# Optimization experiments

Hardware: AMD Instinct MI355X
Metric: run time of the kernel (lower is better)

## Reference

```python
import jax, jax.numpy as jnp
import numpy as np

B, S, H, NH = 2, 2048, 1024, 16
HD = H // NH  # 64
EPS = 1e-5


def setup_inputs() -> dict:
    key = jax.random.key(0)
    ks = jax.random.split(key, 4)
    return {
        "hidden_states": jax.random.normal(ks[0], (B, S, H), dtype=jnp.float32),
        "W_attn": jax.random.normal(ks[1], (H, 3 * H), dtype=jnp.float32) * (1.0 / np.sqrt(H)),
        "b_attn": jnp.zeros((3 * H,), dtype=jnp.float32),
        "W_proj": jax.random.normal(ks[2], (H, H), dtype=jnp.float32) * (1.0 / np.sqrt(H)),
        "b_proj": jnp.zeros((H,), dtype=jnp.float32),
        "q_gamma": jnp.ones((HD,), dtype=jnp.float32),
        "q_beta": jnp.zeros((HD,), dtype=jnp.float32),
        "k_gamma": jnp.ones((HD,), dtype=jnp.float32),
        "k_beta": jnp.zeros((HD,), dtype=jnp.float32),
    }


def _layernorm(x, gamma, beta):
    mu = jnp.mean(x, axis=-1, keepdims=True)
    var = jnp.mean(jnp.square(x - mu), axis=-1, keepdims=True)
    return (x - mu) * jax.lax.rsqrt(var + EPS) * gamma + beta


def reference(hidden_states, W_attn, b_attn, W_proj, b_proj, q_gamma, q_beta, k_gamma, k_beta):
    b, s, h = hidden_states.shape
    qkv = hidden_states @ W_attn + b_attn  # [B,S,3H]
    q, k, v = jnp.split(qkv, 3, axis=-1)
    # [B,S,H] -> [B,NH,S,HD]
    def to_heads(t):
        return t.reshape(b, s, NH, HD).transpose(0, 2, 1, 3)
    q, k, v = to_heads(q), to_heads(k), to_heads(v)
    # QK LayerNorm over head_dim
    q = _layernorm(q, q_gamma, q_beta)
    k = _layernorm(k, k_gamma, k_beta)
    scale = HD ** (-0.5)
    scores = jnp.einsum("bhqd,bhkd->bhqk", q, k) * scale
    causal = jnp.tril(jnp.ones((s, s), dtype=bool))
    mask_value = jnp.finfo(scores.dtype).min
    scores = jnp.where(causal, scores, mask_value)
    attn = jax.nn.softmax(scores.astype(jnp.float32), axis=-1).astype(q.dtype)
    out = jnp.einsum("bhqk,bhkd->bhqd", attn, v)
    out = out.transpose(0, 2, 1, 3).reshape(b, s, h)
    out = out @ W_proj + b_proj
    return out
```

## Files before the change

### kernel.cpp

```cpp
#include <hip/hip_runtime.h>
#include <hip/hip_bf16.h>

typedef __bf16 bf16x8 __attribute__((ext_vector_type(8)));
typedef float f32x4 __attribute__((ext_vector_type(4)));

#define EPS 1e-5f
#define QSCALE 0.18033688011112042f

__device__ __forceinline__ unsigned short f2bf(float f) {
  union { float f; unsigned int i; } c; c.f = f;
  unsigned int r = c.i + 0x7FFFu + ((c.i >> 16) & 1u);
  return (unsigned short)(r >> 16);
}
__device__ __forceinline__ unsigned short f2bf_t(float f) {
  union { float f; unsigned int i; } c; c.f = f;
  return (unsigned short)(c.i >> 16);
}

__device__ __forceinline__ void glds16(const void* g, void* l) {
  __builtin_amdgcn_global_load_lds(
      (const __attribute__((address_space(1))) unsigned int*)g,
      (__attribute__((address_space(3))) unsigned int*)l, 16, 0, 0);
}

__device__ __forceinline__ void transpose_tile(
    const float* __restrict__ in, unsigned short* __restrict__ out,
    int R, int C, int ct0, int rt0, unsigned short* S )
{
  const int t = threadIdx.x;
  const int r = t >> 2, c4 = (t & 3) * 16;
  {
    long base = (long)(rt0 + r) * C + ct0 + c4;
    float4 a = *(const float4*)&in[base];
    float4 b = *(const float4*)&in[base + 4];
    float4 c = *(const float4*)&in[base + 8];
    float4 d = *(const float4*)&in[base + 12];
    unsigned short v[16] = {f2bf(a.x), f2bf(a.y), f2bf(a.z), f2bf(a.w),
                            f2bf(b.x), f2bf(b.y), f2bf(b.z), f2bf(b.w),
                            f2bf(c.x), f2bf(c.y), f2bf(c.z), f2bf(c.w),
                            f2bf(d.x), f2bf(d.y), f2bf(d.z), f2bf(d.w)};
    *(uint4*)&S[r * 72 + c4]     = *(uint4*)&v[0];
    *(uint4*)&S[r * 72 + c4 + 8] = *(uint4*)&v[8];
  }
  __syncthreads();
  unsigned short tmp[16];
#pragma unroll
  for (int j = 0; j < 16; j++) tmp[j] = S[(c4 + j) * 72 + r];
  *(uint4*)&out[(long)(ct0 + r) * R + rt0 + c4]     = *(uint4*)&tmp[0];
  *(uint4*)&out[(long)(ct0 + r) * R + rt0 + c4 + 8] = *(uint4*)&tmp[8];
}

__global__ __launch_bounds__(256) void prep_kernel(
    const float* __restrict__ Wa, const float* __restrict__ Wp,
    const float* __restrict__ X,
    unsigned short* __restrict__ WaT, unsigned short* __restrict__ WpT,
    unsigned short* __restrict__ Xbf)
{
  __shared__ __align__(16) unsigned short S[64 * 72];
  const int id = blockIdx.x;
  if (id < 768) {
    transpose_tile(Wa, WaT, 1024, 3072, (id % 48) * 64, (id / 48) * 64, S);
  } else if (id < 1024) {
    const int i2 = id - 768;
    transpose_tile(Wp, WpT, 1024, 1024, (i2 % 16) * 64, (i2 / 16) * 64, S);
  } else {
    long i = ((long)(id - 1024) * 256 + threadIdx.x) * 16;
    float4 a = *(const float4*)&X[i];
    float4 b = *(const float4*)&X[i + 4];
    float4 c = *(const float4*)&X[i + 8];
    float4 d = *(const float4*)&X[i + 12];
    unsigned short v[16] = {f2bf(a.x), f2bf(a.y), f2bf(a.z), f2bf(a.w),
                            f2bf(b.x), f2bf(b.y), f2bf(b.z), f2bf(b.w),
                            f2bf(c.x), f2bf(c.y), f2bf(c.z), f2bf(c.w),
                            f2bf(d.x), f2bf(d.y), f2bf(d.z), f2bf(d.w)};
    *(uint4*)&Xbf[i]     = *(uint4*)&v[0];
    *(uint4*)&Xbf[i + 8] = *(uint4*)&v[8];
  }
}

__global__ __launch_bounds__(256) void qkvt_kernel(
    const float* __restrict__ Xf,
    const unsigned short* __restrict__ Xbf, int use_xbf,
    const unsigned short* __restrict__ WT,
    const float* __restrict__ bias,
    const float* __restrict__ qg, const float* __restrict__ qb,
    const float* __restrict__ kg, const float* __restrict__ kb,
    unsigned short* __restrict__ Qws, unsigned short* __restrict__ Kws,
    unsigned short* __restrict__ Vt)
{
  __shared__ __align__(16) unsigned short As[2][128 * 32];
  __shared__ __align__(16) unsigned short Bs[2][128 * 32];

  const int tid = threadIdx.x;
  const int w = tid >> 6, lane = tid & 63, quad = lane >> 4, l15 = lane & 15;
  const int mh = w & 1, nh = w >> 1;
  const int id = blockIdx.x;
  const int grow = lane >> 2, gcol = (lane & 3) * 8;

  if (id < 512) {
    const int n0 = (id & 15) * 128, m0 = (id >> 4) * 128;

    f32x4 acc[4][4];
#pragma unroll
    for (int i = 0; i < 4; i++)
#pragma unroll
      for (int j = 0; j < 4; j++) acc[i][j] = (f32x4){0.f, 0.f, 0.f, 0.f};

    if (use_xbf) {
      const long ga = (long)(m0 + w * 32 + grow) * 1024 + gcol;
      const long gb = (long)(n0 + w * 32 + grow) * 1024 + gcol;
#define STAGE_QK(bf, kk) do { \
        glds16(&Xbf[ga + (kk)],             &As[bf][(w * 32) * 32]); \
        glds16(&Xbf[ga + (kk) + 16 * 1024], &As[bf][(w * 32 + 16) * 32]); \
        glds16(&WT[gb + (kk)],              &Bs[bf][(w * 32) * 32]); \
        glds16(&WT[gb + (kk) + 16 * 1024],  &Bs[bf][(w * 32 + 16) * 32]); \
      } while (0)
      STAGE_QK(0, 0);
      __syncthreads();
      int buf = 0;
      for (int kt = 0; kt < 1024; kt += 32) {
        if (kt + 32 < 1024) STAGE_QK(buf ^ 1, kt + 32);
        bf16x8 af[4], bfr[4];
#pragma unroll
        for (int mq = 0; mq < 4; mq++)
          af[mq] = *(const bf16x8*)&As[buf][(mh * 64 + mq * 16 + l15) * 32 + quad * 8];
#pragma unroll
        for (int nq = 0; nq < 4; nq++)
          bfr[nq] = *(const bf16x8*)&Bs[buf][(nh * 64 + nq * 16 + l15) * 32 + quad * 8];
#pragma unroll
        for (int mq = 0; mq < 4; mq++)
#pragma unroll
          for (int nq = 0; nq < 4; nq++)
            acc[mq][nq] = __builtin_amdgcn_mfma_f32_16x16x32_bf16(af[mq], bfr[nq], acc[mq][nq], 0, 0, 0);
        __syncthreads();
        buf ^= 1;
      }
#undef STAGE_QK
    } else {
      const int sr2 = tid >> 1, sh2 = (tid & 1) * 16;
      {
        long xo = (long)(m0 + sr2) * 1024 + sh2;
        float4 a0 = *(const float4*)&Xf[xo];
        float4 a1 = *(const float4*)&Xf[xo + 4];
        float4 a2 = *(const float4*)&Xf[xo + 8];
        float4 a3 = *(const float4*)&Xf[xo + 12];
        unsigned short v[16] = {f2bf(a0.x), f2bf(a0.y), f2bf(a0.z), f2bf(a0.w),
                                f2bf(a1.x), f2bf(a1.y), f2bf(a1.z), f2bf(a1.w),
                                f2bf(a2.x), f2bf(a2.y), f2bf(a2.z), f2bf(a2.w),
                                f2bf(a3.x), f2bf(a3.y), f2bf(a3.z), f2bf(a3.w)};
        *(uint4*)&As[0][sr2 * 32 + sh2]     = *(uint4*)&v[0];
        *(uint4*)&As[0][sr2 * 32 + sh2 + 8] = *(uint4*)&v[8];
        long wo = (long)(n0 + sr2) * 1024 + sh2;
        *(uint4*)&Bs[0][sr2 * 32 + sh2]     = *(const uint4*)&WT[wo];
        *(uint4*)&Bs[0][sr2 * 32 + sh2 + 8] = *(const uint4*)&WT[wo + 8];
      }
      __syncthreads();

      int buf = 0;
      for (int kt = 0; kt < 1024; kt += 32) {
        const int nbuf = buf ^ 1;
        const bool pf = (kt + 32) < 1024;
        uint4 wv0, wv1;
        float4 a0, a1, a2, a3;
        if (pf) {
          long xo = (long)(m0 + sr2) * 1024 + kt + 32 + sh2;
          a0 = *(const float4*)&Xf[xo];
          a1 = *(const float4*)&Xf[xo + 4];
          a2 = *(const float4*)&Xf[xo + 8];
          a3 = *(const float4*)&Xf[xo + 12];
          long wo = (long)(n0 + sr2) * 1024 + kt + 32 + sh2;
          wv0 = *(const uint4*)&WT[wo];
          wv1 = *(const uint4*)&WT[wo + 8];
        }

        bf16x8 af[4], bfr[4];
#pragma unroll
        for (int mq = 0; mq < 4; mq++)
          af[mq] = *(const bf16x8*)&As[buf][(mh * 64 + mq * 16 + l15) * 32 + quad * 8];
#pragma unroll
        for (int nq = 0; nq < 4; nq++)
          bfr[nq] = *(const bf16x8*)&Bs[buf][(nh * 64 + nq * 16 + l15) * 32 + quad * 8];
#pragma unroll
        for (int mq = 0; mq < 4; mq++)
#pragma unroll
          for (int nq = 0; nq < 4; nq++)
            acc[mq][nq] = __builtin_amdgcn_mfma_f32_16x16x32_bf16(af[mq], bfr[nq], acc[mq][nq], 0, 0, 0);

        if (pf) {
          unsigned short v[16] = {f2bf(a0.x), f2bf(a0.y), f2bf(a0.z), f2bf(a0.w),
                                  f2bf(a1.x), f2bf(a1.y), f2bf(a1.z), f2bf(a1.w),
                                  f2bf(a2.x), f2bf(a2.y), f2bf(a2.z), f2bf(a2.w),
                                  f2bf(a3.x), f2bf(a3.y), f2bf(a3.z), f2bf(a3.w)};
          *(uint4*)&As[nbuf][sr2 * 32 + sh2]     = *(uint4*)&v[0];
          *(uint4*)&As[nbuf][sr2 * 32 + sh2 + 8] = *(uint4*)&v[8];
          *(uint4*)&Bs[nbuf][sr2 * 32 + sh2]     = wv0;
          *(uint4*)&Bs[nbuf][sr2 * 32 + sh2 + 8] = wv1;
        }
        __syncthreads();
        buf = nbuf;
      }
    }

#pragma unroll
    for (int nq = 0; nq < 4; nq++) {
      float bv = bias[n0 + nh * 64 + nq * 16 + l15];
#pragma unroll
      for (int mq = 0; mq < 4; mq++)
#pragma unroll
        for (int rr = 0; rr < 4; rr++) acc[mq][nq][rr] += bv;
    }

    const int g = (n0 >> 6) + nh;
    const bool isQ = g < 16;
    {
      float gv[4], bev[4];
#pragma unroll
      for (int nq = 0; nq < 4; nq++) {
        int d = nq * 16 + l15;
        gv[nq]  = isQ ? qg[d] : kg[d];
        bev[nq] = isQ ? qb[d] : kb[d];
        if (isQ) { gv[nq] *= QSCALE; bev[nq] *= QSCALE; }
      }
#pragma unroll
      for (int mq = 0; mq < 4; mq++)
#pragma unroll
        for (int rr = 0; rr < 4; rr++) {
          float s  = acc[mq][0][rr] + acc[mq][1][rr] + acc[mq][2][rr] + acc[mq][3][rr];
          float s2 = acc[mq][0][rr]*acc[mq][0][rr] + acc[mq][1][rr]*acc[mq][1][rr]
                   + acc[mq][2][rr]*acc[mq][2][rr] + acc[mq][3][rr]*acc[mq][3][rr];
#pragma unroll
          for (int off = 1; off < 16; off <<= 1) {
            s  += __shfl_xor(s,  off, 64);
            s2 += __shfl_xor(s2, off, 64);
          }
          float mu   = s * (1.0f / 64.0f);
          float var  = fmaxf(s2 * (1.0f / 64.0f) - mu * mu, 0.f);
          float rstd = rsqrtf(var + EPS);
#pragma unroll
          for (int nq = 0; nq < 4; nq++)
            acc[mq][nq][rr] = (acc[mq][nq][rr] - mu) * rstd * gv[nq] + bev[nq];
        }
    }

    unsigned short* dst = isQ ? Qws : Kws;
    const int head = isQ ? g : g - 16;
#pragma unroll
    for (int mq = 0; mq < 4; mq++)
#pragma unroll
      for (int rr = 0; rr < 4; rr++) {
        int m = m0 + mh * 64 + mq * 16 + quad * 4 + rr;
        int b = m >> 11, s = m & 2047;
        long base = ((long)((b * 16 + head) * 2048 + s)) * 64;
#pragma unroll
        for (int nq = 0; nq < 4; nq++)
          dst[base + nq * 16 + l15] = f2bf(acc[mq][nq][rr]);
      }
  } else {
    const int id2 = id - 512;
    const int n0 = (id2 & 31) * 64, m0 = ((id2 >> 5) & 7) * 128, bz = id2 >> 8;
    const long xrow0 = (long)bz * 2048;
    const unsigned short* WvT = WT + 2048L * 1024;

    f32x4 acc[4][2];
#pragma unroll
    for (int i = 0; i < 4; i++)
#pragma unroll
      for (int j = 0; j < 2; j++) acc[i][j] = (f32x4){0.f, 0.f, 0.f, 0.f};

    if (use_xbf) {
      const long gva = (long)(m0 + w * 32 + grow) * 1024 + gcol;
      const long gvb = (xrow0 + n0 + w * 16 + grow) * 1024 + gcol;
#define STAGE_V(bf, kk) do { \
        glds16(&WvT[gva + (kk)],             &As[bf][(w * 32) * 32]); \
        glds16(&WvT[gva + (kk) + 16 * 1024], &As[bf][(w * 32 + 16) * 32]); \
        glds16(&Xbf[gvb + (kk)],             &Bs[bf][(w * 16) * 32]); \
      } while (0)
      STAGE_V(0, 0);
      __syncthreads();
      int buf = 0;
      for (int kt = 0; kt < 1024; kt += 32) {
        if (kt + 32 < 1024) STAGE_V(buf ^ 1, kt + 32);
        bf16x8 af[4], bfr[2];
#pragma unroll
        for (int mq = 0; mq < 4; mq++)
          af[mq] = *(const bf16x8*)&As[buf][(mh * 64 + mq * 16 + l15) * 32 + quad * 8];
#pragma unroll
        for (int nq = 0; nq < 2; nq++)
          bfr[nq] = *(const bf16x8*)&Bs[buf][(nh * 32 + nq * 16 + l15) * 32 + quad * 8];
#pragma unroll
        for (int mq = 0; mq < 4; mq++)
#pragma unroll
          for (int nq = 0; nq < 2; nq++)
            acc[mq][nq] = __builtin_amdgcn_mfma_f32_16x16x32_bf16(af[mq], bfr[nq], acc[mq][nq], 0, 0, 0);
        __syncthreads();
        buf ^= 1;
      }
#undef STAGE_V
    } else {
      const int srA = tid >> 1, shA = (tid & 1) * 16;
      const int srB = tid >> 2, shB = (tid & 3) * 8;
      {
        long wo = (long)(m0 + srA) * 1024 + shA;
        *(uint4*)&As[0][srA * 32 + shA]     = *(const uint4*)&WvT[wo];
        *(uint4*)&As[0][srA * 32 + shA + 8] = *(const uint4*)&WvT[wo + 8];
        long xo = (xrow0 + n0 + srB) * 1024 + shB;
        float4 a0 = *(const float4*)&Xf[xo];
        float4 a1 = *(const float4*)&Xf[xo + 4];
        unsigned short v[8] = {f2bf(a0.x), f2bf(a0.y), f2bf(a0.z), f2bf(a0.w),
                               f2bf(a1.x), f2bf(a1.y), f2bf(a1.z), f2bf(a1.w)};
        *(uint4*)&Bs[0][srB * 32 + shB] = *(uint4*)v;
      }
      __syncthreads();

      int buf = 0;
      for (int kt = 0; kt < 1024; kt += 32) {
        const int nbuf = buf ^ 1;
        const bool pf = (kt + 32) < 1024;
        uint4 wv0, wv1;
        float4 a0, a1;
        if (pf) {
          long wo = (long)(m0 + srA) * 1024 + kt + 32 + shA;
          wv0 = *(const uint4*)&WvT[wo];
          wv1 = *(const uint4*)&WvT[wo + 8];
          long xo = (xrow0 + n0 + srB) * 1024 + kt + 32 + shB;
          a0 = *(const float4*)&Xf[xo];
          a1 = *(const float4*)&Xf[xo + 4];
        }

        bf16x8 af[4], bfr[2];
#pragma unroll
        for (int mq = 0; mq < 4; mq++)
          af[mq] = *(const bf16x8*)&As[buf][(mh * 64 + mq * 16 + l15) * 32 + quad * 8];
#pragma unroll
        for (int nq = 0; nq < 2; nq++)
          bfr[nq] = *(const bf16x8*)&Bs[buf][(nh * 32 + nq * 16 + l15) * 32 + quad * 8];
#pragma unroll
        for (int mq = 0; mq < 4; mq++)
#pragma unroll
          for (int nq = 0; nq < 2; nq++)
            acc[mq][nq] = __builtin_amdgcn_mfma_f32_16x16x32_bf16(af[mq], bfr[nq], acc[mq][nq], 0, 0, 0);

        if (pf) {
          *(uint4*)&As[nbuf][srA * 32 + shA]     = wv0;
          *(uint4*)&As[nbuf][srA * 32 + shA + 8] = wv1;
          unsigned short v[8] = {f2bf(a0.x), f2bf(a0.y), f2bf(a0.z), f2bf(a0.w),
                                 f2bf(a1.x), f2bf(a1.y), f2bf(a1.z), f2bf(a1.w)};
          *(uint4*)&Bs[nbuf][srB * 32 + shB] = *(uint4*)v;
        }
        __syncthreads();
        buf = nbuf;
      }
    }

    const long outb = (long)bz * 2097152;
#pragma unroll
    for (int mq = 0; mq < 4; mq++)
#pragma unroll
      for (int rr = 0; rr < 4; rr++) {
        int m = m0 + mh * 64 + mq * 16 + quad * 4 + rr;
        float bv = bias[2048 + m];
#pragma unroll
        for (int nq = 0; nq < 2; nq++) {
          int n = n0 + nh * 32 + nq * 16 + l15;
          Vt[outb + (long)m * 2048 + n] = f2bf(acc[mq][nq][rr] + bv);
        }
      }
  }
}

__global__ __launch_bounds__(512) void attn_kernel(
    unsigned short* __restrict__ Qws,
    const unsigned short* __restrict__ Kws,
    const unsigned short* __restrict__ Vt)
{
  __shared__ __align__(16) unsigned short Ks[2][64 * 72];
  __shared__ __align__(16) unsigned short VTs[2][64 * 72];
  __shared__ __align__(16) unsigned short Ps[2][64 * 64];

  const int tid = threadIdx.x;
  const int w = tid >> 6, lane = tid & 63, quad = lane >> 4, l15 = lane & 15;
  const int g = w >> 2, wq = w & 3;
  const int id = blockIdx.x;
  const int bh = (id & 7) * 4 + ((id >> 3) & 3);
  const int i5 = id >> 5;
  const int x  = (i5 < 8) ? i5 : 23 - i5;
  const long bhoff = (long)bh * 2048 * 64;
  const long bhv   = (long)bh * 131072;

  const int qt_long = 31 - x;
  const int myqt  = g ? x : qt_long;
  const int qbase = myqt * 64;
  const int jsteps = qt_long + 1;

  const int t2 = tid & 255;
  const int sr = t2 >> 2, sc = (t2 & 3) * 16;
  const int qsw = ((sr >> 2) & 3) << 4;
  const int sw = ((l15 >> 2) & 3) << 4;
  const int pc0 = (quad * 8) ^ sw;
  const int pc1 = (32 + quad * 8) ^ sw;

  bf16x8 ones;
  {
    union { unsigned short u[8]; bf16x8 v; } c;
#pragma unroll
    for (int i = 0; i < 8; i++) c.u[i] = 0x3F80u;
    ones = c.v;
  }

  *(uint4*)&Ps[g][sr * 64 + (sc ^ qsw)]       = *(const uint4*)&Qws[bhoff + (qbase + sr) * 64 + sc];
  *(uint4*)&Ps[g][sr * 64 + ((sc ^ qsw) + 8)] = *(const uint4*)&Qws[bhoff + (qbase + sr) * 64 + sc + 8];
  if (g == 0) {
    *(uint4*)&Ks[0][sr * 72 + sc]      = *(const uint4*)&Kws[bhoff + sr * 64 + sc];
    *(uint4*)&Ks[0][sr * 72 + sc + 8]  = *(const uint4*)&Kws[bhoff + sr * 64 + sc + 8];
  } else {
    *(uint4*)&VTs[0][sr * 72 + sc]     = *(const uint4*)&Vt[bhv + sr * 2048 + sc];
    *(uint4*)&VTs[0][sr * 72 + sc + 8] = *(const uint4*)&Vt[bhv + sr * 2048 + sc + 8];
  }
  __syncthreads();

  const bf16x8 qf0 = *(const bf16x8*)&Ps[g][(wq * 16 + l15) * 64 + pc0];
  const bf16x8 qf1 = *(const bf16x8*)&Ps[g][(wq * 16 + l15) * 64 + pc1];

  f32x4 o[4], osum;
#pragma unroll
  for (int i = 0; i < 4; i++) o[i] = (f32x4){0.f, 0.f, 0.f, 0.f};
  osum = (f32x4){0.f, 0.f, 0.f, 0.f};

  int cb = 0;
  for (int j = 0; j < jsteps; j++) {
    const int kb = j * 64;
    const bool pf = (j + 1) < jsteps;
    uint4 p0, p1;
    if (pf) {
      const int kb1 = kb + 64;
      if (g == 0) {
        p0 = *(const uint4*)&Kws[bhoff + (kb1 + sr) * 64 + sc];
        p1 = *(const uint4*)&Kws[bhoff + (kb1 + sr) * 64 + sc + 8];
      } else {
        p0 = *(const uint4*)&Vt[bhv + sr * 2048 + kb1 + sc];
        p1 = *(const uint4*)&Vt[bhv + sr * 2048 + kb1 + sc + 8];
      }
    }

    if (j <= myqt) {
      f32x4 sacc[4];
#pragma unroll
      for (int i = 0; i < 4; i++) sacc[i] = (f32x4){0.f, 0.f, 0.f, 0.f};
#pragma unroll
      for (int nt = 0; nt < 4; nt++) {
        bf16x8 kf0 = *(const bf16x8*)&Ks[cb][(nt * 16 + l15) * 72 + quad * 8];
        bf16x8 kf1 = *(const bf16x8*)&Ks[cb][(nt * 16 + l15) * 72 + 32 + quad * 8];
        sacc[nt] = __builtin_amdgcn_mfma_f32_16x16x32_bf16(qf0, kf0, sacc[nt], 0, 0, 0);
        sacc[nt] = __builtin_amdgcn_mfma_f32_16x16x32_bf16(qf1, kf1, sacc[nt], 0, 0, 0);
      }

      const bool domask = (j == myqt);
#pragma unroll
      for (int nt = 0; nt < 4; nt++)
#pragma unroll
        for (int rr = 0; rr < 4; rr++) {
          float p = exp2f(sacc[nt][rr]);
          if (domask) {
            int kcol = kb + nt * 16 + l15;
            int qrow = qbase + wq * 16 + quad * 4 + rr;
            if (kcol > qrow) p = 0.f;
          }
          sacc[nt][rr] = p;
        }

#pragma unroll
      for (int rr = 0; rr < 4; rr++)
#pragma unroll
        for (int nt = 0; nt < 4; nt++)
          Ps[g][(wq * 16 + quad * 4 + rr) * 64 + (((nt ^ quad) & 3) * 16 + l15)]
              = f2bf_t(sacc[nt][rr]);

      bf16x8 pfr0 = *(const bf16x8*)&Ps[g][(wq * 16 + l15) * 64 + pc0];
      bf16x8 pfr1 = *(const bf16x8*)&Ps[g][(wq * 16 + l15) * 64 + pc1];

      osum = __builtin_amdgcn_mfma_f32_16x16x32_bf16(pfr0, ones, osum, 0, 0, 0);
      osum = __builtin_amdgcn_mfma_f32_16x16x32_bf16(pfr1, ones, osum, 0, 0, 0);
#pragma unroll
      for (int dt = 0; dt < 4; dt++) {
        bf16x8 vf0 = *(const bf16x8*)&VTs[cb][(dt * 16 + l15) * 72 + quad * 8];
        bf16x8 vf1 = *(const bf16x8*)&VTs[cb][(dt * 16 + l15) * 72 + 32 + quad * 8];
        o[dt] = __builtin_amdgcn_mfma_f32_16x16x32_bf16(pfr0, vf0, o[dt], 0, 0, 0);
        o[dt] = __builtin_amdgcn_mfma_f32_16x16x32_bf16(pfr1, vf1, o[dt], 0, 0, 0);
      }
    }

    if (pf) {
      const int nb = cb ^ 1;
      if (g == 0) {
        *(uint4*)&Ks[nb][sr * 72 + sc]      = p0;
        *(uint4*)&Ks[nb][sr * 72 + sc + 8]  = p1;
      } else {
        *(uint4*)&VTs[nb][sr * 72 + sc]     = p0;
        *(uint4*)&VTs[nb][sr * 72 + sc + 8] = p1;
      }
      __syncthreads();
      cb = nb;
    }
  }

#pragma unroll
  for (int rr = 0; rr < 4; rr++) {
    float inv = 1.0f / osum[rr];
    int row = qbase + wq * 16 + quad * 4 + rr;
    long base = bhoff + (long)row * 64;
#pragma unroll
    for (int dt = 0; dt < 4; dt++)
      Qws[base + dt * 16 + l15] = f2bf(o[dt][rr] * inv);
  }
}

__global__ __launch_bounds__(256) void proj_kernel(
    const unsigned short* __restrict__ AQ,
    const unsigned short* __restrict__ WT,
    const float* __restrict__ bias,
    float* __restrict__ Out)
{
  __shared__ __align__(16) unsigned short As[2][128 * 32];
  __shared__ __align__(16) unsigned short Bs[2][64 * 32];

  const int tid = threadIdx.x;
  const int w = tid >> 6, lane = tid & 63, quad = lane >> 4, l15 = lane & 15;
  const int mh = w & 1, nh = w >> 1;
  const int n0 = blockIdx.x * 64, m0 = blockIdx.y * 128;

  f32x4 acc[4][2];
#pragma unroll
  for (int i = 0; i < 4; i++)
#pragma unroll
    for (int j = 0; j < 2; j++) acc[i][j] = (f32x4){0.f, 0.f, 0.f, 0.f};

  const int srA = tid >> 1, shA = (tid & 1) * 16;
  const int srB = tid >> 2, shB = (tid & 3) * 8;
  const int m = m0 + srA, b = m >> 11, s = m & 2047;

  {
    const int h = shA >> 6, d = shA & 63;
    long ao = ((long)((b * 16 + h) * 2048 + s)) * 64 + d;
    *(uint4*)&As[0][srA * 32 + shA]     = *(const uint4*)&AQ[ao];
    *(uint4*)&As[0][srA * 32 + shA + 8] = *(const uint4*)&AQ[ao + 8];
    long wo = (long)(n0 + srB) * 1024 + shB;
    *(uint4*)&Bs[0][srB * 32 + shB] = *(const uint4*)&WT[wo];
  }
  __syncthreads();

  int buf = 0;
  for (int kt = 0; kt < 1024; kt += 32) {
    const int nbuf = buf ^ 1;
    const bool pf = (kt + 32) < 1024;
    uint4 av0, av1, wv0;
    if (pf) {
      const int k = kt + 32 + shA, h = k >> 6, d = k & 63;
      long ao = ((long)((b * 16 + h) * 2048 + s)) * 64 + d;
      av0 = *(const uint4*)&AQ[ao];
      av1 = *(const uint4*)&AQ[ao + 8];
      long wo = (long)(n0 + srB) * 1024 + kt + 32 + shB;
      wv0 = *(const uint4*)&WT[wo];
    }

    bf16x8 af[4], bfr[2];
#pragma unroll
    for (int mq = 0; mq < 4; mq++)
      af[mq] = *(const bf16x8*)&As[buf][(mh * 64 + mq * 16 + l15) * 32 + quad * 8];
#pragma unroll
    for (int nq = 0; nq < 2; nq++)
      bfr[nq] = *(const bf16x8*)&Bs[buf][(nh * 32 + nq * 16 + l15) * 32 + quad * 8];
#pragma unroll
    for (int mq = 0; mq < 4; mq++)
#pragma unroll
      for (int nq = 0; nq < 2; nq++)
        acc[mq][nq] = __builtin_amdgcn_mfma_f32_16x16x32_bf16(af[mq], bfr[nq], acc[mq][nq], 0, 0, 0);

    if (pf) {
      *(uint4*)&As[nbuf][srA * 32 + shA]     = av0;
      *(uint4*)&As[nbuf][srA * 32 + shA + 8] = av1;
      *(uint4*)&Bs[nbuf][srB * 32 + shB]     = wv0;
    }
    __syncthreads();
    buf = nbuf;
  }

#pragma unroll
  for (int nq = 0; nq < 2; nq++) {
    int n = n0 + nh * 32 + nq * 16 + l15;
    float bv = bias[n];
#pragma unroll
    for (int mq = 0; mq < 4; mq++)
#pragma unroll
      for (int rr = 0; rr < 4; rr++) {
        int mm = m0 + mh * 64 + mq * 16 + quad * 4 + rr;
        Out[(long)mm * 1024 + n] = acc[mq][nq][rr] + bv;
      }
  }
}

extern "C" void kernel_launch(void* const* d_in, const int* in_sizes, int n_in,
                              void* d_out, int out_size, void* d_ws, size_t ws_size,
                              hipStream_t stream) {
  const float* X  = (const float*)d_in[0];
  const float* Wa = (const float*)d_in[1];
  const float* ba = (const float*)d_in[2];
  const float* Wp = (const float*)d_in[3];
  const float* bp = (const float*)d_in[4];
  const float* qg = (const float*)d_in[5];
  const float* qb = (const float*)d_in[6];
  const float* kg = (const float*)d_in[7];
  const float* kb = (const float*)d_in[8];

  const long per = 2L * 16 * 2048 * 64;
  unsigned short* ws  = (unsigned short*)d_ws;
  unsigned short* Qws = ws;
  unsigned short* Kws = Qws + per;
  unsigned short* Vt  = Kws + per;

  const bool big = ws_size >= (size_t)(5L * per * 2);
  unsigned short *Xbf, *WaT, *WpT;
  if (big) {
    Xbf = Vt + per;
    WaT = Xbf + per;
    WpT = WaT + 3072L * 1024;
  } else {
    Xbf = Qws;
    WaT = Vt + per;
    WpT = WaT + 3072L * 1024;
  }

  prep_kernel<<<big ? 2048 : 1024, 256, 0, stream>>>(Wa, Wp, X, WaT, WpT, Xbf);
  qkvt_kernel<<<1024, 256, 0, stream>>>(X, Xbf, big ? 1 : 0, WaT, ba,
                                        qg, qb, kg, kb, Qws, Kws, Vt);
  attn_kernel<<<512, 512, 0, stream>>>(Qws, Kws, Vt);
  proj_kernel<<<dim3(16, 32), 256, 0, stream>>>(Qws, WpT, bp, (float*)d_out);
}
```

Measured before the change: 205.9 us.

## Add 256x256-tile 8-wave QKV GEMM with swizzled LDS and XCD-aware block mapping

Adds a new QKV projection kernel for the big-workspace path. It uses 256x256 output tiles, 512 threads, K-steps of 64, and direct global-to-LDS loads with XOR-swizzled LDS addresses. MFMA work is split into phases interleaved with prefetches, using explicit waitcnt and barriers plus s_setprio. Block IDs are remapped so neighbouring tiles land on the same XCD, and proj_kernel gets the same XCD-aware 1D mapping. The aim is more operand reuse, fewer LDS bank conflicts and better L2 locality, at the cost of a large LDS footprint (128KB) and occupancy of one block per CU.

```diff
diff --git a/kernel.cpp b/kernel.cpp
--- a/kernel.cpp
+++ b/kernel.cpp
@@ -78,9 +78,221 @@
   }
 }
 
+__global__ __launch_bounds__(512) void qkvt8_kernel(
+    const unsigned short* __restrict__ Xbf,
+    const unsigned short* __restrict__ WT,
+    const float* __restrict__ bias,
+    const float* __restrict__ qg, const float* __restrict__ qb,
+    const float* __restrict__ kg, const float* __restrict__ kb,
+    unsigned short* __restrict__ Qws, unsigned short* __restrict__ Kws,
+    unsigned short* __restrict__ Vt)
+{
+  __shared__ __align__(16) unsigned short As[2][256 * 64];
+  __shared__ __align__(16) unsigned short Bs[2][256 * 64];
+
+  const int tid = threadIdx.x;
+  const int wv = tid >> 6, lane = tid & 63, quad = lane >> 4, l15 = lane & 15;
+  const int wm = wv >> 2, wn = wv & 3;
+  const int id = blockIdx.x;
+
+  const unsigned short *Abase, *Bbase;
+  int m0, n0, bz = 0;
+  bool isV;
+  if (id < 128) {
+    const int xcd = id & 7, lid = id >> 3;
+    m0 = (((xcd >> 1) << 2) + (lid >> 2)) * 256;
+    n0 = (((xcd & 1) << 2) + (lid & 3)) * 256;
+    Abase = Xbf; Bbase = WT; isV = false;
+  } else {
+    const int vid = id - 128, xcd = vid & 7, lid2 = vid >> 3;
+    bz = xcd >> 2;
+    n0 = (((xcd & 3) << 1) + (lid2 & 1)) * 256;
+    m0 = (lid2 >> 1) * 256;
+    Abase = WT + 2048L * 1024;
+    Bbase = Xbf + (long)bz * 2048 * 1024;
+    isV = true;
+  }
+
+  const int gsw  = ((lane & 7) ^ (((lane >> 5) & 1) << 1)) * 8;
+  const int grow = lane >> 3;
+  const int rsw = (l15 & 4) >> 1;
+  const int co0 = ((0 + quad) ^ rsw) * 8;
+  const int co1 = ((4 + quad) ^ rsw) * 8;
+
+#define STG_A(BUF, H, KK) do { \
+    const int L0_ = wv * 2, L1_ = L0_ + 1; \
+    const int r0_ = ((L0_ >> 3) << 7) + (H) * 64 + ((L0_ & 7) << 3); \
+    const int r1_ = ((L1_ >> 3) << 7) + (H) * 64 + ((L1_ & 7) << 3); \
+    glds16(&Abase[(long)(m0 + r0_ + grow) * 1024 + (KK) + gsw], &As[BUF][r0_ * 64]); \
+    glds16(&Abase[(long)(m0 + r1_ + grow) * 1024 + (KK) + gsw], &As[BUF][r1_ * 64]); \
+  } while (0)
+#define STG_B(BUF, H, KK) do { \
+    const int L0_ = wv * 2, L1_ = L0_ + 1; \
+    const int r0_ = ((L0_ >> 2) << 6) + (H) * 32 + ((L0_ & 3) << 3); \
+    const int r1_ = ((L1_ >> 2) << 6) + (H) * 32 + ((L1_ & 3) << 3); \
+    glds16(&Bbase[(long)(n0 + r0_ + grow) * 1024 + (KK) + gsw], &Bs[BUF][r0_ * 64]); \
+    glds16(&Bbase[(long)(n0 + r1_ + grow) * 1024 + (KK) + gsw], &Bs[BUF][r1_ * 64]); \
+  } while (0)
+#define LDA4(BUF, MQB) \
+  _Pragma("unroll") \
+  for (int q = 0; q < 4; q++) { \
+    const int r_ = (wm * 128 + ((MQB) + q) * 16 + l15) * 64; \
+    a[q][0] = *(const bf16x8*)&As[BUF][r_ + co0]; \
+    a[q][1] = *(const bf16x8*)&As[BUF][r_ + co1]; \
+  }
+#define LDB2(BUF, NQB, DST) \
+  _Pragma("unroll") \
+  for (int q = 0; q < 2; q++) { \
+    const int r_ = (wn * 64 + ((NQB) + q) * 16 + l15) * 64; \
+    DST[q][0] = *(const bf16x8*)&Bs[BUF][r_ + co0]; \
+    DST[q][1] = *(const bf16x8*)&Bs[BUF][r_ + co1]; \
+  }
+#define MMQ(MQB, NQB, BV) \
+  __builtin_amdgcn_s_setprio(1); \
+  _Pragma("unroll") \
+  for (int qi = 0; qi < 4; qi++) \
+    _Pragma("unroll") \
+    for (int qj = 0; qj < 2; qj++) { \
+      acc[(MQB) + qi][(NQB) + qj] = __builtin_amdgcn_mfma_f32_16x16x32_bf16( \
+          a[qi][0], BV[qj][0], acc[(MQB) + qi][(NQB) + qj], 0, 0, 0); \
+      acc[(MQB) + qi][(NQB) + qj] = __builtin_amdgcn_mfma_f32_16x16x32_bf16( \
+          a[qi][1], BV[qj][1], acc[(MQB) + qi][(NQB) + qj], 0, 0, 0); \
+    } \
+  __builtin_amdgcn_s_setprio(0)
+#define PH_MID() do { __builtin_amdgcn_s_barrier(); \
+    asm volatile("s_waitcnt lgkmcnt(0)" ::: "memory"); } while (0)
+#define PH_END() __builtin_amdgcn_s_barrier()
+
+  f32x4 acc[8][4];
+#pragma unroll
+  for (int i = 0; i < 8; i++)
+#pragma unroll
+    for (int j = 0; j < 4; j++) acc[i][j] = (f32x4){0.f, 0.f, 0.f, 0.f};
+
+  STG_A(0, 0, 0); STG_B(0, 0, 0); STG_B(0, 1, 0); STG_A(0, 1, 0);
+  STG_A(1, 0, 64); STG_B(1, 0, 64); STG_B(1, 1, 64);
+  asm volatile("s_waitcnt vmcnt(6)" ::: "memory");
+  __builtin_amdgcn_s_barrier();
+
+  for (int it = 0; it < 8; it++) {
+    const int k1 = it * 128 + 64;
+    const int k2 = it * 128 + 128;
+    const int k3 = it * 128 + 192;
+    const bool pf = (it < 7);
+    bf16x8 a[4][2], b01[2][2], b23[2][2];
+
+    LDA4(0, 0) LDB2(0, 0, b01)
+    STG_A(1, 1, k1);
+    PH_MID(); MMQ(0, 0, b01); PH_END();
+    LDB2(0, 2, b23)
+    if (pf) STG_A(0, 0, k2);
+    PH_MID(); MMQ(0, 2, b23); PH_END();
+    LDA4(0, 4)
+    if (pf) STG_B(0, 0, k2);
+    PH_MID(); MMQ(4, 2, b23); PH_END();
+    if (pf) { STG_B(0, 1, k2);
+      asm volatile("s_waitcnt vmcnt(6)" ::: "memory");
+    } else {
+      asm volatile("s_waitcnt vmcnt(0)" ::: "memory");
+    }
+    PH_MID(); MMQ(4, 0, b01); PH_END();
+
+    LDA4(1, 0) LDB2(1, 0, b01)
+    if (pf) STG_A(0, 1, k2);
+    PH_MID(); MMQ(0, 0, b01); PH_END();
+    LDB2(1, 2, b23)
+    if (pf) STG_A(1, 0, k3);
+    PH_MID(); MMQ(0, 2, b23); PH_END();
+    LDA4(1, 4)
+    if (pf) STG_B(1, 0, k3);
+    PH_MID(); MMQ(4, 2, b23); PH_END();
+    if (pf) { STG_B(1, 1, k3);
+      asm volatile("s_waitcnt vmcnt(6)" ::: "memory");
+    } else {
+      asm volatile("s_waitcnt vmcnt(0)" ::: "memory");
+    }
+    PH_MID(); MMQ(4, 0, b01); PH_END();
+  }
+#undef STG_A
+#undef STG_B
+#undef LDA4
+#undef LDB2
+#undef MMQ
+#undef PH_MID
+#undef PH_END
+
+  if (!isV) {
+#pragma unroll
+    for (int nq = 0; nq < 4; nq++) {
+      float bv = bias[n0 + wn * 64 + nq * 16 + l15];
+#pragma unroll
+      for (int mq = 0; mq < 8; mq++)
+#pragma unroll
+        for (int rr = 0; rr < 4; rr++) acc[mq][nq][rr] += bv;
+    }
+
+    const int g = (n0 >> 6) + wn;
+    const bool isQ = g < 16;
+    float gv[4], bev[4];
+#pragma unroll
+    for (int nq = 0; nq < 4; nq++) {
+      int d = nq * 16 + l15;
+      gv[nq]  = isQ ? qg[d] : kg[d];
+      bev[nq] = isQ ? qb[d] : kb[d];
+      if (isQ) { gv[nq] *= QSCALE; bev[nq] *= QSCALE; }
+    }
+#pragma unroll
+    for (int mq = 0; mq < 8; mq++)
+#pragma unroll
+      for (int rr = 0; rr < 4; rr++) {
+        float s  = acc[mq][0][rr] + acc[mq][1][rr] + acc[mq][2][rr] + acc[mq][3][rr];
+        float s2 = acc[mq][0][rr]*acc[mq][0][rr] + acc[mq][1][rr]*acc[mq][1][rr]
+                 + acc[mq][2][rr]*acc[mq][2][rr] + acc[mq][3][rr]*acc[mq][3][rr];
+#pragma unroll
+        for (int off = 1; off < 16; off <<= 1) {
+          s  += __shfl_xor(s,  off, 64);
+          s2 += __shfl_xor(s2, off, 64);
+        }
+        float mu   = s * (1.0f / 64.0f);
+        float var  = fmaxf(s2 * (1.0f / 64.0f) - mu * mu, 0.f);
+        float rstd = rsqrtf(var + EPS);
+#pragma unroll
+        for (int nq = 0; nq < 4; nq++)
+          acc[mq][nq][rr] = (acc[mq][nq][rr] - mu) * rstd * gv[nq] + bev[nq];
+      }
+
+    unsigned short* dst = isQ ? Qws : Kws;
+    const int head = isQ ? g : g - 16;
+#pragma unroll
+    for (int mq = 0; mq < 8; mq++)
+#pragma unroll
+      for (int rr = 0; rr < 4; rr++) {
+        int m = m0 + wm * 128 + mq * 16 + quad * 4 + rr;
+        int b = m >> 11, s = m & 2047;
+        long base = ((long)((b * 16 + head) * 2048 + s)) * 64;
+#pragma unroll
+        for (int nq = 0; nq < 4; nq++)
+          dst[base + nq * 16 + l15] = f2bf(acc[mq][nq][rr]);
+      }
+  } else {
+    const long outb = (long)bz * 2097152;
+#pragma unroll
+    for (int mq = 0; mq < 8; mq++)
+#pragma unroll
+      for (int rr = 0; rr < 4; rr++) {
+        int m = m0 + wm * 128 + mq * 16 + quad * 4 + rr;
+        float bv = bias[2048 + m];
+#pragma unroll
+        for (int nq = 0; nq < 4; nq++) {
+          int n = n0 + wn * 64 + nq * 16 + l15;
+          Vt[outb + (long)m * 2048 + n] = f2bf(acc[mq][nq][rr] + bv);
+        }
+      }
+  }
+}
+
 __global__ __launch_bounds__(256) void qkvt_kernel(
     const float* __restrict__ Xf,
-    const unsigned short* __restrict__ Xbf, int use_xbf,
     const unsigned short* __restrict__ WT,
     const float* __restrict__ bias,
     const float* __restrict__ qg, const float* __restrict__ qb,
@@ -95,110 +307,74 @@
   const int w = tid >> 6, lane = tid & 63, quad = lane >> 4, l15 = lane & 15;
   const int mh = w & 1, nh = w >> 1;
   const int id = blockIdx.x;
-  const int grow = lane >> 2, gcol = (lane & 3) * 8;
 
   if (id < 512) {
     const int n0 = (id & 15) * 128, m0 = (id >> 4) * 128;
-
     f32x4 acc[4][4];
 #pragma unroll
     for (int i = 0; i < 4; i++)
 #pragma unroll
       for (int j = 0; j < 4; j++) acc[i][j] = (f32x4){0.f, 0.f, 0.f, 0.f};
 
-    if (use_xbf) {
-      const long ga = (long)(m0 + w * 32 + grow) * 1024 + gcol;
-      const long gb = (long)(n0 + w * 32 + grow) * 1024 + gcol;
-#define STAGE_QK(bf, kk) do { \
-        glds16(&Xbf[ga + (kk)],             &As[bf][(w * 32) * 32]); \
-        glds16(&Xbf[ga + (kk) + 16 * 1024], &As[bf][(w * 32 + 16) * 32]); \
-        glds16(&WT[gb + (kk)],              &Bs[bf][(w * 32) * 32]); \
-        glds16(&WT[gb + (kk) + 16 * 1024],  &Bs[bf][(w * 32 + 16) * 32]); \
-      } while (0)
-      STAGE_QK(0, 0);
-      __syncthreads();
-      int buf = 0;
-      for (int kt = 0; kt < 1024; kt += 32) {
-        if (kt + 32 < 1024) STAGE_QK(buf ^ 1, kt + 32);
-        bf16x8 af[4], bfr[4];
-#pragma unroll
-        for (int mq = 0; mq < 4; mq++)
-          af[mq] = *(const bf16x8*)&As[buf][(mh * 64 + mq * 16 + l15) * 32 + quad * 8];
+    const int sr2 = tid >> 1, sh2 = (tid & 1) * 16;
+    {
+      long xo = (long)(m0 + sr2) * 1024 + sh2;
+      float4 a0 = *(const float4*)&Xf[xo];
+      float4 a1 = *(const float4*)&Xf[xo + 4];
+      float4 a2 = *(const float4*)&Xf[xo + 8];
+      float4 a3 = *(const float4*)&Xf[xo + 12];
+      unsigned short v[16] = {f2bf(a0.x), f2bf(a0.y), f2bf(a0.z), f2bf(a0.w),
+                              f2bf(a1.x), f2bf(a1.y), f2bf(a1.z), f2bf(a1.w),
+                              f2bf(a2.x), f2bf(a2.y), f2bf(a2.z), f2bf(a2.w),
+                              f2bf(a3.x), f2bf(a3.y), f2bf(a3.z), f2bf(a3.w)};
+      *(uint4*)&As[0][sr2 * 32 + sh2]     = *(uint4*)&v[0];
+      *(uint4*)&As[0][sr2 * 32 + sh2 + 8] = *(uint4*)&v[8];
+      long wo = (long)(n0 + sr2) * 1024 + sh2;
+      *(uint4*)&Bs[0][sr2 * 32 + sh2]     = *(const uint4*)&WT[wo];
+      *(uint4*)&Bs[0][sr2 * 32 + sh2 + 8] = *(const uint4*)&WT[wo + 8];
+    }
+    __syncthreads();
+
+    int buf = 0;
+    for (int kt = 0; kt < 1024; kt += 32) {
+      const int nbuf = buf ^ 1;
+      const bool pf = (kt + 32) < 1024;
+      uint4 wv0, wv1;
+      float4 a0, a1, a2, a3;
+      if (pf) {
+        long xo = (long)(m0 + sr2) * 1024 + kt + 32 + sh2;
+        a0 = *(const float4*)&Xf[xo];
+        a1 = *(const float4*)&Xf[xo + 4];
+        a2 = *(const float4*)&Xf[xo + 8];
+        a3 = *(const float4*)&Xf[xo + 12];
+        long wo = (long)(n0 + sr2) * 1024 + kt + 32 + sh2;
+        wv0 = *(const uint4*)&WT[wo];
+        wv1 = *(const uint4*)&WT[wo + 8];
+      }
+      bf16x8 af[4], bfr[4];
+#pragma unroll
+      for (int mq = 0; mq < 4; mq++)
+        af[mq] = *(const bf16x8*)&As[buf][(mh * 64 + mq * 16 + l15) * 32 + quad * 8];
+#pragma unroll
+      for (int nq = 0; nq < 4; nq++)
+        bfr[nq] = *(const bf16x8*)&Bs[buf][(nh * 64 + nq * 16 + l15) * 32 + quad * 8];
+#pragma unroll
+      for (int mq = 0; mq < 4; mq++)
 #pragma unroll
         for (int nq = 0; nq < 4; nq++)
-          bfr[nq] = *(const bf16x8*)&Bs[buf][(nh * 64 + nq * 16 + l15) * 32 + quad * 8];
-#pragma unroll
-        for (int mq = 0; mq < 4; mq++)
-#pragma unroll
-          for (int nq = 0; nq < 4; nq++)
-            acc[mq][nq] = __builtin_amdgcn_mfma_f32_16x16x32_bf16(af[mq], bfr[nq], acc[mq][nq], 0, 0, 0);
-        __syncthreads();
-        buf ^= 1;
-      }
-#undef STAGE_QK
-    } else {
-      const int sr2 = tid >> 1, sh2 = (tid & 1) * 16;
-      {
-        long xo = (long)(m0 + sr2) * 1024 + sh2;
-        float4 a0 = *(const float4*)&Xf[xo];
-        float4 a1 = *(const float4*)&Xf[xo + 4];
-        float4 a2 = *(const float4*)&Xf[xo + 8];
-        float4 a3 = *(const float4*)&Xf[xo + 12];
+          acc[mq][nq] = __builtin_amdgcn_mfma_f32_16x16x32_bf16(af[mq], bfr[nq], acc[mq][nq], 0, 0, 0);
+      if (pf) {
         unsigned short v[16] = {f2bf(a0.x), f2bf(a0.y), f2bf(a0.z), f2bf(a0.w),
                                 f2bf(a1.x), f2bf(a1.y), f2bf(a1.z), f2bf(a1.w),
                                 f2bf(a2.x), f2bf(a2.y), f2bf(a2.z), f2bf(a2.w),
                                 f2bf(a3.x), f2bf(a3.y), f2bf(a3.z), f2bf(a3.w)};
-        *(uint4*)&As[0][sr2 * 32 + sh2]     = *(uint4*)&v[0];
-        *(uint4*)&As[0][sr2 * 32 + sh2 + 8] = *(uint4*)&v[8];
-        long wo = (long)(n0 + sr2) * 1024 + sh2;
-        *(uint4*)&Bs[0][sr2 * 32 + sh2]     = *(const uint4*)&WT[wo];
-        *(uint4*)&Bs[0][sr2 * 32 + sh2 + 8] = *(const uint4*)&WT[wo + 8];
+        *(uint4*)&As[nbuf][sr2 * 32 + sh2]     = *(uint4*)&v[0];
+        *(uint4*)&As[nbuf][sr2 * 32 + sh2 + 8] = *(uint4*)&v[8];
+        *(uint4*)&Bs[nbuf][sr2 * 32 + sh2]     = wv0;
+        *(uint4*)&Bs[nbuf][sr2 * 32 + sh2 + 8] = wv1;
       }
       __syncthreads();
-
-      int buf = 0;
-      for (int kt = 0; kt < 1024; kt += 32) {
-        const int nbuf = buf ^ 1;
-        const bool pf = (kt + 32) < 1024;
-        uint4 wv0, wv1;
-        float4 a0, a1, a2, a3;
-        if (pf) {
-          long xo = (long)(m0 + sr2) * 1024 + kt + 32 + sh2;
-          a0 = *(const float4*)&Xf[xo];
-          a1 = *(const float4*)&Xf[xo + 4];
-          a2 = *(const float4*)&Xf[xo + 8];
-          a3 = *(const float4*)&Xf[xo + 12];
-          long wo = (long)(n0 + sr2) * 1024 + kt + 32 + sh2;
-          wv0 = *(const uint4*)&WT[wo];
-          wv1 = *(const uint4*)&WT[wo + 8];
-        }
-
-        bf16x8 af[4], bfr[4];
-#pragma unroll
-        for (int mq = 0; mq < 4; mq++)
-          af[mq] = *(const bf16x8*)&As[buf][(mh * 64 + mq * 16 + l15) * 32 + quad * 8];
-#pragma unroll
-        for (int nq = 0; nq < 4; nq++)
-          bfr[nq] = *(const bf16x8*)&Bs[buf][(nh * 64 + nq * 16 + l15) * 32 + quad * 8];
-#pragma unroll
-        for (int mq = 0; mq < 4; mq++)
-#pragma unroll
-          for (int nq = 0; nq < 4; nq++)
-            acc[mq][nq] = __builtin_amdgcn_mfma_f32_16x16x32_bf16(af[mq], bfr[nq], acc[mq][nq], 0, 0, 0);
-
-        if (pf) {
-          unsigned short v[16] = {f2bf(a0.x), f2bf(a0.y), f2bf(a0.z), f2bf(a0.w),
-                                  f2bf(a1.x), f2bf(a1.y), f2bf(a1.z), f2bf(a1.w),
-                                  f2bf(a2.x), f2bf(a2.y), f2bf(a2.z), f2bf(a2.w),
-                                  f2bf(a3.x), f2bf(a3.y), f2bf(a3.z), f2bf(a3.w)};
-          *(uint4*)&As[nbuf][sr2 * 32 + sh2]     = *(uint4*)&v[0];
-          *(uint4*)&As[nbuf][sr2 * 32 + sh2 + 8] = *(uint4*)&v[8];
-          *(uint4*)&Bs[nbuf][sr2 * 32 + sh2]     = wv0;
-          *(uint4*)&Bs[nbuf][sr2 * 32 + sh2 + 8] = wv1;
-        }
-        __syncthreads();
-        buf = nbuf;
-      }
+      buf = nbuf;
     }
 
 #pragma unroll
@@ -209,7 +385,6 @@
 #pragma unroll
         for (int rr = 0; rr < 4; rr++) acc[mq][nq][rr] += bv;
     }
-
     const int g = (n0 >> 6) + nh;
     const bool isQ = g < 16;
     {
@@ -241,7 +416,6 @@
             acc[mq][nq][rr] = (acc[mq][nq][rr] - mu) * rstd * gv[nq] + bev[nq];
         }
     }
-
     unsigned short* dst = isQ ? Qws : Kws;
     const int head = isQ ? g : g - 16;
 #pragma unroll
@@ -267,89 +441,56 @@
 #pragma unroll
       for (int j = 0; j < 2; j++) acc[i][j] = (f32x4){0.f, 0.f, 0.f, 0.f};
 
-    if (use_xbf) {
-      const long gva = (long)(m0 + w * 32 + grow) * 1024 + gcol;
-      const long gvb = (xrow0 + n0 + w * 16 + grow) * 1024 + gcol;
-#define STAGE_V(bf, kk) do { \
-        glds16(&WvT[gva + (kk)],             &As[bf][(w * 32) * 32]); \
-        glds16(&WvT[gva + (kk) + 16 * 1024], &As[bf][(w * 32 + 16) * 32]); \
-        glds16(&Xbf[gvb + (kk)],             &Bs[bf][(w * 16) * 32]); \
-      } while (0)
-      STAGE_V(0, 0);
-      __syncthreads();
-      int buf = 0;
-      for (int kt = 0; kt < 1024; kt += 32) {
-        if (kt + 32 < 1024) STAGE_V(buf ^ 1, kt + 32);
-        bf16x8 af[4], bfr[2];
-#pragma unroll
-        for (int mq = 0; mq < 4; mq++)
-          af[mq] = *(const bf16x8*)&As[buf][(mh * 64 + mq * 16 + l15) * 32 + quad * 8];
+    const int srA = tid >> 1, shA = (tid & 1) * 16;
+    const int srB = tid >> 2, shB = (tid & 3) * 8;
+    {
+      long wo = (long)(m0 + srA) * 1024 + shA;
+      *(uint4*)&As[0][srA * 32 + shA]     = *(const uint4*)&WvT[wo];
+      *(uint4*)&As[0][srA * 32 + shA + 8] = *(const uint4*)&WvT[wo + 8];
+      long xo = (xrow0 + n0 + srB) * 1024 + shB;
+      float4 a0 = *(const float4*)&Xf[xo];
+      float4 a1 = *(const float4*)&Xf[xo + 4];
+      unsigned short v[8] = {f2bf(a0.x), f2bf(a0.y), f2bf(a0.z), f2bf(a0.w),
+                             f2bf(a1.x), f2bf(a1.y), f2bf(a1.z), f2bf(a1.w)};
+      *(uint4*)&Bs[0][srB * 32 + shB] = *(uint4*)v;
+    }
+    __syncthreads();
+
+    int buf = 0;
+    for (int kt = 0; kt < 1024; kt += 32) {
+      const int nbuf = buf ^ 1;
+      const bool pf = (kt + 32) < 1024;
+      uint4 wv0, wv1;
+      float4 a0, a1;
+      if (pf) {
+        long wo = (long)(m0 + srA) * 1024 + kt + 32 + shA;
+        wv0 = *(const uint4*)&WvT[wo];
+        wv1 = *(const uint4*)&WvT[wo + 8];
+        long xo = (xrow0 + n0 + srB) * 1024 + kt + 32 + shB;
+        a0 = *(const float4*)&Xf[xo];
+        a1 = *(const float4*)&Xf[xo + 4];
+      }
+      bf16x8 af[4], bfr[2];
+#pragma unroll
+      for (int mq = 0; mq < 4; mq++)
+        af[mq] = *(const bf16x8*)&As[buf][(mh * 64 + mq * 16 + l15) * 32 + quad * 8];
+#pragma unroll
+      for (int nq = 0; nq < 2; nq++)
+        bfr[nq] = *(const bf16x8*)&Bs[buf][(nh * 32 + nq * 16 + l15) * 32 + quad * 8];
+#pragma unroll
+      for (int mq = 0; mq < 4; mq++)
 #pragma unroll
         for (int nq = 0; nq < 2; nq++)
-          bfr[nq] = *(const bf16x8*)&Bs[buf][(nh * 32 + nq * 16 + l15) * 32 + quad * 8];
-#pragma unroll
-        for (int mq = 0; mq < 4; mq++)
-#pragma unroll
-          for (int nq = 0; nq < 2; nq++)
-            acc[mq][nq] = __builtin_amdgcn_mfma_f32_16x16x32_bf16(af[mq], bfr[nq], acc[mq][nq], 0, 0, 0);
-        __syncthreads();
-        buf ^= 1;
-      }
-#undef STAGE_V
-    } else {
-      const int srA = tid >> 1, shA = (tid & 1) * 16;
-      const int srB = tid >> 2, shB = (tid & 3) * 8;
-      {
-        long wo = (long)(m0 + srA) * 1024 + shA;
-        *(uint4*)&As[0][srA * 32 + shA]     = *(const uint4*)&WvT[wo];
-        *(uint4*)&As[0][srA * 32 + shA + 8] = *(const uint4*)&WvT[wo + 8];
-        long xo = (xrow0 + n0 + srB) * 1024 + shB;
-        float4 a0 = *(const float4*)&Xf[xo];
-        float4 a1 = *(const float4*)&Xf[xo + 4];
+          acc[mq][nq] = __builtin_amdgcn_mfma_f32_16x16x32_bf16(af[mq], bfr[nq], acc[mq][nq], 0, 0, 0);
+      if (pf) {
+        *(uint4*)&As[nbuf][srA * 32 + shA]     = wv0;
+        *(uint4*)&As[nbuf][srA * 32 + shA + 8] = wv1;
         unsigned short v[8] = {f2bf(a0.x), f2bf(a0.y), f2bf(a0.z), f2bf(a0.w),
                                f2bf(a1.x), f2bf(a1.y), f2bf(a1.z), f2bf(a1.w)};
-        *(uint4*)&Bs[0][srB * 32 + shB] = *(uint4*)v;
+        *(uint4*)&Bs[nbuf][srB * 32 + shB] = *(uint4*)v;
       }
       __syncthreads();
-
-      int buf = 0;
-      for (int kt = 0; kt < 1024; kt += 32) {
-        const int nbuf = buf ^ 1;
-        const bool pf = (kt + 32) < 1024;
-        uint4 wv0, wv1;
-        float4 a0, a1;
-        if (pf) {
-          long wo = (long)(m0 + srA) * 1024 + kt + 32 + shA;
-          wv0 = *(const uint4*)&WvT[wo];
-          wv1 = *(const uint4*)&WvT[wo + 8];
-          long xo = (xrow0 + n0 + srB) * 1024 + kt + 32 + shB;
-          a0 = *(const float4*)&Xf[xo];
-          a1 = *(const float4*)&Xf[xo + 4];
-        }
-
-        bf16x8 af[4], bfr[2];
-#pragma unroll
-        for (int mq = 0; mq < 4; mq++)
-          af[mq] = *(const bf16x8*)&As[buf][(mh * 64 + mq * 16 + l15) * 32 + quad * 8];
-#pragma unroll
-        for (int nq = 0; nq < 2; nq++)
-          bfr[nq] = *(const bf16x8*)&Bs[buf][(nh * 32 + nq * 16 + l15) * 32 + quad * 8];
-#pragma unroll
-        for (int mq = 0; mq < 4; mq++)
-#pragma unroll
-          for (int nq = 0; nq < 2; nq++)
-            acc[mq][nq] = __builtin_amdgcn_mfma_f32_16x16x32_bf16(af[mq], bfr[nq], acc[mq][nq], 0, 0, 0);
-
-        if (pf) {
-          *(uint4*)&As[nbuf][srA * 32 + shA]     = wv0;
-          *(uint4*)&As[nbuf][srA * 32 + shA + 8] = wv1;
-          unsigned short v[8] = {f2bf(a0.x), f2bf(a0.y), f2bf(a0.z), f2bf(a0.w),
-                                 f2bf(a1.x), f2bf(a1.y), f2bf(a1.z), f2bf(a1.w)};
-          *(uint4*)&Bs[nbuf][srB * 32 + shB] = *(uint4*)v;
-        }
-        __syncthreads();
-        buf = nbuf;
-      }
+      buf = nbuf;
     }
 
     const long outb = (long)bz * 2097152;
@@ -526,7 +667,10 @@
   const int tid = threadIdx.x;
   const int w = tid >> 6, lane = tid & 63, quad = lane >> 4, l15 = lane & 15;
   const int mh = w & 1, nh = w >> 1;
-  const int n0 = blockIdx.x * 64, m0 = blockIdx.y * 128;
+  const int id = blockIdx.x;
+  const int xcd = id & 7, lid = id >> 3;
+  const int m0 = (((xcd >> 1) << 3) + (lid >> 3)) * 128;
+  const int n0 = (((xcd & 1) << 3) + (lid & 7)) * 64;
 
   f32x4 acc[4][2];
 #pragma unroll
@@ -630,8 +774,13 @@
   }
 
   prep_kernel<<<big ? 2048 : 1024, 256, 0, stream>>>(Wa, Wp, X, WaT, WpT, Xbf);
-  qkvt_kernel<<<1024, 256, 0, stream>>>(X, Xbf, big ? 1 : 0, WaT, ba,
-                                        qg, qb, kg, kb, Qws, Kws, Vt);
+  if (big) {
+    qkvt8_kernel<<<192, 512, 0, stream>>>(Xbf, WaT, ba, qg, qb, kg, kb,
+                                          Qws, Kws, Vt);
+  } else {
+    qkvt_kernel<<<1024, 256, 0, stream>>>(X, WaT, ba, qg, qb, kg, kb,
+                                          Qws, Kws, Vt);
+  }
   attn_kernel<<<512, 512, 0, stream>>>(Qws, Kws, Vt);
-  proj_kernel<<<dim3(16, 32), 256, 0, stream>>>(Qws, WpT, bp, (float*)d_out);
-}
+  proj_kernel<<<512, 256, 0, stream>>>(Qws, WpT, bp, (float*)d_out);
+}
```

Result: slower. 221.4 us (+7.5%).

## Give each attention block one contiguous 128-row query tile instead of paired tiles

Applied to the files above, without the earlier changes.

The attention kernel previously paired a short and a long 64-row query tile per block for load balance. Both 256-thread groups walked the long tile's K/V range, so the short-tile group sat idle for most iterations. Now each block owns a contiguous 128-row query range. Its two halves share almost the same K/V steps, which cuts redundant K/V tile loads and idle waves. In exchange, per-block work now varies with t (2 to 32 steps), which relies on the block ordering and hardware scheduling to keep CUs balanced.

```diff
diff --git a/kernel.cpp b/kernel.cpp
--- a/kernel.cpp
+++ b/kernel.cpp
@@ -375,26 +375,26 @@
 {
   __shared__ __align__(16) unsigned short Ks[2][64 * 72];
   __shared__ __align__(16) unsigned short VTs[2][64 * 72];
-  __shared__ __align__(16) unsigned short Ps[2][64 * 64];
+  __shared__ __align__(16) unsigned short Ps[128 * 64];
 
   const int tid = threadIdx.x;
   const int w = tid >> 6, lane = tid & 63, quad = lane >> 4, l15 = lane & 15;
-  const int g = w >> 2, wq = w & 3;
+  const int g = w >> 2;
   const int id = blockIdx.x;
   const int bh = (id & 7) * 4 + ((id >> 3) & 3);
   const int i5 = id >> 5;
-  const int x  = (i5 < 8) ? i5 : 23 - i5;
+  const int t  = (i5 < 8) ? i5 : 23 - i5;
   const long bhoff = (long)bh * 2048 * 64;
   const long bhv   = (long)bh * 131072;
 
-  const int qt_long = 31 - x;
-  const int myqt  = g ? x : qt_long;
-  const int qbase = myqt * 64;
-  const int jsteps = qt_long + 1;
-
+  const int qbase  = t * 128;
+  const int jsteps = 2 * t + 2;
+  const int dj     = 2 * t + g;
+
+  const int qr = tid >> 2, qc = (tid & 3) * 16;
+  const int qsw = ((qr >> 2) & 3) << 4;
   const int t2 = tid & 255;
   const int sr = t2 >> 2, sc = (t2 & 3) * 16;
-  const int qsw = ((sr >> 2) & 3) << 4;
   const int sw = ((l15 >> 2) & 3) << 4;
   const int pc0 = (quad * 8) ^ sw;
   const int pc1 = (32 + quad * 8) ^ sw;
@@ -407,8 +407,8 @@
     ones = c.v;
   }
 
-  *(uint4*)&Ps[g][sr * 64 + (sc ^ qsw)]       = *(const uint4*)&Qws[bhoff + (qbase + sr) * 64 + sc];
-  *(uint4*)&Ps[g][sr * 64 + ((sc ^ qsw) + 8)] = *(const uint4*)&Qws[bhoff + (qbase + sr) * 64 + sc + 8];
+  *(uint4*)&Ps[qr * 64 + (qc ^ qsw)]       = *(const uint4*)&Qws[bhoff + (qbase + qr) * 64 + qc];
+  *(uint4*)&Ps[qr * 64 + ((qc ^ qsw) + 8)] = *(const uint4*)&Qws[bhoff + (qbase + qr) * 64 + qc + 8];
   if (g == 0) {
     *(uint4*)&Ks[0][sr * 72 + sc]      = *(const uint4*)&Kws[bhoff + sr * 64 + sc];
     *(uint4*)&Ks[0][sr * 72 + sc + 8]  = *(const uint4*)&Kws[bhoff + sr * 64 + sc + 8];
@@ -418,8 +418,8 @@
   }
   __syncthreads();
 
-  const bf16x8 qf0 = *(const bf16x8*)&Ps[g][(wq * 16 + l15) * 64 + pc0];
-  const bf16x8 qf1 = *(const bf16x8*)&Ps[g][(wq * 16 + l15) * 64 + pc1];
+  const bf16x8 qf0 = *(const bf16x8*)&Ps[(w * 16 + l15) * 64 + pc0];
+  const bf16x8 qf1 = *(const bf16x8*)&Ps[(w * 16 + l15) * 64 + pc1];
 
   f32x4 o[4], osum;
 #pragma unroll
@@ -442,7 +442,7 @@
       }
     }
 
-    if (j <= myqt) {
+    if (j <= dj) {
       f32x4 sacc[4];
 #pragma unroll
       for (int i = 0; i < 4; i++) sacc[i] = (f32x4){0.f, 0.f, 0.f, 0.f};
@@ -454,7 +454,7 @@
         sacc[nt] = __builtin_amdgcn_mfma_f32_16x16x32_bf16(qf1, kf1, sacc[nt], 0, 0, 0);
       }
 
-      const bool domask = (j == myqt);
+      const bool domask = (j == dj);
 #pragma unroll
       for (int nt = 0; nt < 4; nt++)
 #pragma unroll
@@ -462,7 +462,7 @@
           float p = exp2f(sacc[nt][rr]);
           if (domask) {
             int kcol = kb + nt * 16 + l15;
-            int qrow = qbase + wq * 16 + quad * 4 + rr;
+            int qrow = qbase + w * 16 + quad * 4 + rr;
             if (kcol > qrow) p = 0.f;
           }
           sacc[nt][rr] = p;
@@ -472,11 +472,11 @@
       for (int rr = 0; rr < 4; rr++)
 #pragma unroll
         for (int nt = 0; nt < 4; nt++)
-          Ps[g][(wq * 16 + quad * 4 + rr) * 64 + (((nt ^ quad) & 3) * 16 + l15)]
+          Ps[(w * 16 + quad * 4 + rr) * 64 + (((nt ^ quad) & 3) * 16 + l15)]
               = f2bf_t(sacc[nt][rr]);
 
-      bf16x8 pfr0 = *(const bf16x8*)&Ps[g][(wq * 16 + l15) * 64 + pc0];
-      bf16x8 pfr1 = *(const bf16x8*)&Ps[g][(wq * 16 + l15) * 64 + pc1];
+      bf16x8 pfr0 = *(const bf16x8*)&Ps[(w * 16 + l15) * 64 + pc0];
+      bf16x8 pfr1 = *(const bf16x8*)&Ps[(w * 16 + l15) * 64 + pc1];
 
       osum = __builtin_amdgcn_mfma_f32_16x16x32_bf16(pfr0, ones, osum, 0, 0, 0);
       osum = __builtin_amdgcn_mfma_f32_16x16x32_bf16(pfr1, ones, osum, 0, 0, 0);
@@ -506,7 +506,7 @@
 #pragma unroll
   for (int rr = 0; rr < 4; rr++) {
     float inv = 1.0f / osum[rr];
-    int row = qbase + wq * 16 + quad * 4 + rr;
+    int row = qbase + w * 16 + quad * 4 + rr;
     long base = bhoff + (long)row * 64;
 #pragma unroll
     for (int dt = 0; dt < 4; dt++)
```

After: 210.1 us. 1.02x slower.
